# Performance work log

Hardware: AMD Instinct MI355X
Metric: run time of the kernel (lower is better)

Reference implementation:

```python
import jax, jax.numpy as jnp
import numpy as np

B, IC, OC, K, H, W = 8, 512, 512, 3, 32, 32
GAIN, LRMUL = 1.0, 1.0
# compute_runtime_coef: fan_in = prod(weight_shape[:-1])
RC_CONV = GAIN / np.sqrt(K * K * IC) * LRMUL   # conv weight [K,K,IC,OC]
RC_DENSE = GAIN / np.sqrt(IC) * LRMUL          # dense weight [IC, IC]


def setup_inputs() -> dict:
    key = jax.random.key(0)
    ks = jax.random.split(key, 4)
    x = jax.random.normal(ks[0], (B, IC, H, W), dtype=jnp.float32)
    w = jax.random.normal(ks[1], (B, IC), dtype=jnp.float32)
    # init_std = 1/lrmul = 1.0 for both weights; bias init zeros
    conv_w = jax.random.normal(ks[2], (K, K, IC, OC), dtype=jnp.float32)
    dense_w = jax.random.normal(ks[3], (IC, IC), dtype=jnp.float32)
    dense_b = jnp.zeros((IC,), dtype=jnp.float32)
    return {"x": x, "w": w, "conv_w": conv_w, "dense_w": dense_w, "dense_b": dense_b}


def reference(x, w, conv_w, dense_w, dense_b):
    b, ic, h, wd = x.shape
    # modulation: style = Dense(w) + bias + 1
    style = w @ (RC_DENSE * dense_w) + LRMUL * dense_b + 1.0        # [B, IC]
    wt = (RC_CONV * conv_w)[None] * style[:, None, None, :, None]   # [B,K,K,IC,OC]
    # demodulation: rsqrt of sum of squares over (kh, kw, ic)
    d = jax.lax.rsqrt(jnp.sum(jnp.square(wt), axis=(1, 2, 3)) + 1e-8)  # [B, OC]
    wt = wt * d[:, None, None, None, :]
    # grouped conv with groups = batch: weight -> OIHW [B*OC, IC, K, K]
    w_g = jnp.transpose(wt, (0, 4, 3, 1, 2)).reshape(b * OC, ic, K, K)
    xg = x.reshape(1, b * ic, h, wd)
    y = jax.lax.conv_general_dilated(
        xg, w_g, window_strides=(1, 1), padding="SAME",
        dimension_numbers=("NCHW", "OIHW", "NCHW"), feature_group_count=b)
    return y.reshape(b, OC, h, wd)
```

## Files before the change

### kernel.cpp

```cpp
#include <hip/hip_runtime.h>
#include <stdint.h>


#define B_   8
#define IC_  512
#define OC_  512

static constexpr float RC_DENSE = 0.04419417382415922f;
static constexpr float RC_CONV  = 0.014731391274719739f;

typedef _Float16 half8    __attribute__((ext_vector_type(8)));
typedef float    floatx16 __attribute__((ext_vector_type(16)));

__device__ __forceinline__ void g2l(const void* g, void* l) {
  __builtin_amdgcn_global_load_lds(
      (const __attribute__((address_space(1))) void*)g,
      (__attribute__((address_space(3))) void*)l, 16, 0, 0);
}

__global__ __launch_bounds__(256) void style_kernel(
    const float* __restrict__ wv, const float* __restrict__ dw,
    const float* __restrict__ db, float* __restrict__ sm,
    float* __restrict__ sm2) {
  const int b = blockIdx.y;
  const int i = blockIdx.x * 64 + (threadIdx.x & 63);
  const int jg = threadIdx.x >> 6;
  __shared__ float red[4][64];
  float p = 0.f;
  for (int j = jg * 128; j < jg * 128 + 128; ++j)
    p += wv[b * IC_ + j] * dw[(size_t)j * IC_ + i];
  red[jg][threadIdx.x & 63] = p;
  __syncthreads();
  if (threadIdx.x < 64) {
    float s = red[0][threadIdx.x] + red[1][threadIdx.x] +
              red[2][threadIdx.x] + red[3][threadIdx.x];
    s = s * RC_DENSE + db[i] + 1.0f;
    float v = s * RC_CONV;
    sm[b * IC_ + i] = v;
    sm2[b * IC_ + i] = v * v;
  }
}

__global__ __launch_bounds__(256) void prep_kernel(
    const float* __restrict__ cw, const float* __restrict__ x,
    const float* __restrict__ sm, const float* __restrict__ sm2,
    _Float16* __restrict__ Wtf, float* __restrict__ dpart,
    _Float16* __restrict__ xsp) {
  __shared__ __align__(16) char smem[33280];
  const int bid = blockIdx.x;
  const int tid = threadIdx.x;
  if (bid < 256) {
    _Float16* LA = (_Float16*)smem;
    float* redall = (float*)(smem + 18432);
    const int by2 = bid >> 4, icb = bid & 15;
    const int by = by2 >> 1, h2 = by2 & 1;
    const int oc0 = by * 64 + h2 * 32, ic0 = icb * 32;
    const int ocl = tid & 31, g = tid >> 5;
    float sq4[4] = {};
    for (int m = 0; m < 36; ++m) {
      int r = m * 8 + g;
      int t = r >> 5, icl = r & 31;
      float v = cw[(size_t)(t * IC_ + ic0 + icl) * OC_ + oc0 + ocl];
      sq4[m & 3] += v * v;
      LA[m * 256 + ocl * 8 + g] = (_Float16)v;
    }
    for (int b = 0; b < 8; ++b) {
      float p = 0.f;
      for (int s = 0; s < 4; ++s)
        p += sm2[b * IC_ + ic0 + g + 8 * s] * sq4[s];
      redall[(b * 8 + g) * 32 + ocl] = p;
    }
    __syncthreads();
    _Float16* dst = Wtf + (size_t)(by * 16 + icb) * 18432;
    for (int it = 0; it < 5; ++it) {
      int c = it * 256 + tid;
      if (c < 1152) {
        int m = c >> 5, o2 = c & 31;
        *(half8*)(dst + (size_t)(m * 64 + h2 * 32 + o2) * 8) =
            *(const half8*)&LA[m * 256 + o2 * 8];
      }
    }
    const int bb = tid >> 5, o3 = tid & 31;
    float s = 0.f;
    for (int g2 = 0; g2 < 8; ++g2) s += redall[(bb * 8 + g2) * 32 + o3];
    dpart[(size_t)icb * 4096 + bb * OC_ + oc0 + o3] = s;
  } else {
    _Float16* Xt = (_Float16*)smem;
    const int rb = bid - 256;
    const int b = rb >> 5, h = rb & 31;
    for (int k = 0; k < 16; ++k) {
      int idx = k * 256 + tid;
      int ic = idx >> 3, wc = (idx & 7) * 4;
      float4 v = *(const float4*)&x[((size_t)(b * IC_ + ic) * 32 + h) * 32 + wc];
      float s = sm[b * IC_ + ic];
      Xt[(wc + 0) * 520 + ic] = (_Float16)(v.x * s);
      Xt[(wc + 1) * 520 + ic] = (_Float16)(v.y * s);
      Xt[(wc + 2) * 520 + ic] = (_Float16)(v.z * s);
      Xt[(wc + 3) * 520 + ic] = (_Float16)(v.w * s);
    }
    __syncthreads();
    _Float16* xb = xsp + (size_t)b * 16 * 36992;
    const int r = h + 1;
    half8 z = {};
    for (int it = 0; it < 9; ++it) {
      int c = it * 256 + tid;
      if (c < 2176) {
        int icb = c / 136, rem = c - 136 * icb, kkq = rem / 34, C = rem - 34 * kkq;
        half8 val = z;
        if (C != 0 && C != 33)
          val = *(const half8*)&Xt[(C - 1) * 520 + icb * 32 + kkq * 8];
        *(half8*)&xb[(size_t)icb * 36992 + (size_t)r * 1088 + kkq * 272 + C * 8] = val;
      }
    }
    if (h == 0 || h == 31) {
      const int rz = (h == 0) ? 0 : 33;
      for (int it = 0; it < 9; ++it) {
        int c = it * 256 + tid;
        if (c < 2176) {
          int icb = c / 136, rem = c - 136 * icb, kkq = rem / 34, C = rem - 34 * kkq;
          *(half8*)&xb[(size_t)icb * 36992 + (size_t)rz * 1088 + kkq * 272 + C * 8] = z;
        }
      }
    }
  }
}

__global__ __launch_bounds__(512, 1) void conv_kernel(
    const _Float16* __restrict__ Wtf,
    const _Float16* __restrict__ xsp,
    const float* __restrict__ dpart,
    float* __restrict__ out) {
  extern __shared__ __align__(16) _Float16 dyn[];
  _Float16* As0 = dyn;
  _Float16* As1 = dyn + 18432;
  _Float16* Xs0 = dyn + 36864;
  _Float16* Xs1 = dyn + 47744;
  float* redd = (float*)(dyn + 58624);
  float* dvl  = redd + 512;

  const int by = blockIdx.x, bx = blockIdx.y, b = blockIdx.z;
  const int tid = threadIdx.x, lane = tid & 63, w = tid >> 6;
  const int wm = w & 1, wn = w >> 1;
  const int n = lane & 31, kq = lane >> 5;
  const int h0 = bx * 8;

  const _Float16* gA = Wtf + (size_t)(by * 16) * 18432;
  const _Float16* gX = xsp + (size_t)b * 16 * 36992 + (size_t)h0 * 1088;

  auto stage = [&](int icb, int p) {
    const _Float16* a  = gA + (size_t)icb * 18432;
    const _Float16* xg = gX + (size_t)icb * 36992;
    _Float16* Ad = p ? As1 : As0;
    _Float16* Xd = p ? Xs1 : Xs0;
#pragma unroll
    for (int k = 0; k < 4; ++k) {
      int c = w * 288 + k * 64 + lane;
      g2l(a + (size_t)c * 8, Ad + c * 8);
    }
    {
      int c = w * 288 + 256 + lane;
      if (lane < 32) g2l(a + (size_t)c * 8, Ad + c * 8);
    }
#pragma unroll
    for (int k = 0; k < 2; ++k) {
      int c = w * 170 + k * 64 + lane;
      g2l(xg + (size_t)c * 8, Xd + c * 8);
    }
    {
      int c = w * 170 + 128 + lane;
      if (lane < 42) g2l(xg + (size_t)c * 8, Xd + c * 8);
    }
  };

  floatx16 acc[2] = {};
  stage(0, 0);
  for (int st = 0; st < 16; ++st) {
    const int cur = st & 1;
    if (st + 1 < 16) {
      stage(st + 1, cur ^ 1);
      __builtin_amdgcn_sched_barrier(0);
      asm volatile("s_waitcnt vmcnt(8)" ::: "memory");
    } else {
      __builtin_amdgcn_sched_barrier(0);
      asm volatile("s_waitcnt vmcnt(0)" ::: "memory");
    }
    __builtin_amdgcn_s_barrier();
    __builtin_amdgcn_sched_barrier(0);
    const _Float16* Ar = (cur ? As1 : As0) + kq * 512 + wm * 256 + n * 8;
    const _Float16* Xr = (cur ? Xs1 : Xs0) + (2 * wn) * 1088 + kq * 272 + n * 8;
    half8 a[9][2];
#pragma unroll
    for (int t = 0; t < 9; ++t) {
      a[t][0] = *(const half8*)(Ar + (t * 4 + 0) * 512);
      a[t][1] = *(const half8*)(Ar + (t * 4 + 2) * 512);
    }
    __builtin_amdgcn_s_setprio(1);
#pragma unroll
    for (int kk = 0; kk < 2; ++kk) {
#pragma unroll
      for (int s = 0; s < 4; ++s) {
#pragma unroll
        for (int kw = 0; kw < 3; ++kw) {
          half8 xv = *(const half8*)(Xr + s * 1088 + kk * 544 + kw * 8);
#pragma unroll
          for (int kh = 0; kh < 3; ++kh) {
            int j = s - kh;
            if (j >= 0 && j < 2)
              acc[j] = __builtin_amdgcn_mfma_f32_32x32x16_f16(
                  a[kh * 3 + kw][kk], xv, acc[j], 0, 0, 0);
          }
        }
      }
    }
    __builtin_amdgcn_s_setprio(0);
    __builtin_amdgcn_sched_barrier(0);
    __builtin_amdgcn_s_barrier();
  }

  const int oc0 = by * 64 + wm * 32;
  __syncthreads();
  {
    const int oc_l = tid & 63, ig = tid >> 6;
    float s = dpart[(size_t)(ig * 2) * 4096 + b * OC_ + by * 64 + oc_l] +
              dpart[(size_t)(ig * 2 + 1) * 4096 + b * OC_ + by * 64 + oc_l];
    redd[ig * 64 + oc_l] = s;
  }
  __syncthreads();
  if (tid < 64) {
    float s = 1e-8f;
#pragma unroll
    for (int g = 0; g < 8; ++g) s += redd[g * 64 + tid];
    dvl[tid] = rsqrtf(s);
  }
  __syncthreads();
  const int r0 = h0 + 2 * wn;
#pragma unroll
  for (int rg = 0; rg < 16; ++rg) {
    const int row = (rg & 3) + 8 * (rg >> 2) + 4 * kq;
    const float dv = dvl[wm * 32 + row];
    float* op = out + ((size_t)b * OC_ + oc0 + row) * 1024 + r0 * 32 + n;
    op[0]  = acc[0][rg] * dv;
    op[32] = acc[1][rg] * dv;
  }
}

extern "C" void kernel_launch(void* const* d_in, const int* in_sizes, int n_in,
                              void* d_out, int out_size, void* d_ws, size_t ws_size,
                              hipStream_t stream) {
  const float* x       = (const float*)d_in[0];
  const float* w       = (const float*)d_in[1];
  const float* conv_w  = (const float*)d_in[2];
  const float* dense_w = (const float*)d_in[3];
  const float* dense_b = (const float*)d_in[4];
  float* out = (float*)d_out;

  char* ws = (char*)d_ws;
  float*    sm    = (float*)ws;
  float*    sm2   = (float*)(ws + (16 << 10));
  float*    dpart = (float*)(ws + (32 << 10));
  _Float16* Wtf   = (_Float16*)(ws + (288 << 10));
  _Float16* xsp   = (_Float16*)(ws + (288 << 10) + 4718592);

  static int dyn_set = 0;
  if (!dyn_set) {
    hipFuncSetAttribute((const void*)conv_kernel,
                        hipFuncAttributeMaxDynamicSharedMemorySize, 119552);
    dyn_set = 1;
  }

  style_kernel<<<dim3(8, B_), 256, 0, stream>>>(w, dense_w, dense_b, sm, sm2);
  prep_kernel<<<512, 256, 0, stream>>>(conv_w, x, sm, sm2, Wtf, dpart, xsp);
  conv_kernel<<<dim3(8, 4, B_), 512, 119552, stream>>>(Wtf, xsp, dpart, out);
}
```

Baseline: 129.3 us.

## Split conv mainloop into finer-grained multi-stage pipeline with interleaved LDS loads

Restructures the conv kernel's mainloop from a two-stage double buffer over whole IC blocks into a deeper pipeline over half-blocks (kk halves). Each block is now processed in four phases. Each phase issues a global-to-LDS copy for a stage ahead, preloads A/X fragments into registers, then runs its MFMAs, with waitcnt tuned per phase. The aim is to overlap memory transfers with MFMA work more evenly and shrink the register footprint of A fragments. The cost is more barriers per block and complex manual vmcnt bookkeeping that could race if miscounted.

```diff
diff --git a/kernel.cpp b/kernel.cpp
--- a/kernel.cpp
+++ b/kernel.cpp
@@ -125,16 +125,59 @@
   }
 }
 
+
+#define VM10 asm volatile("s_waitcnt vmcnt(10)" ::: "memory")
+#define VM5  asm volatile("s_waitcnt vmcnt(5)" ::: "memory")
+#define VM0  asm volatile("s_waitcnt vmcnt(0)" ::: "memory")
+#define VMNONE ((void)0)
+
+#define PHASE(KK, SH, PAR, DO_A, G2L_STMT, VM_STMT)                          \
+  {                                                                          \
+    if (DO_A) {                                                              \
+      const _Float16* Ad = dyn + ((KK) * 2 + (PAR)) * 9216 +                 \
+                           kq * 512 + wm * 256 + n * 8;                      \
+      _Pragma("unroll")                                                      \
+      for (int t_ = 0; t_ < 9; ++t_)                                         \
+        av[t_] = *(const half8*)(Ad + (t_ * 2) * 512);                       \
+    }                                                                        \
+    const _Float16* Xd = XB + ((KK) * 2 + (PAR)) * 5440 +                    \
+                         (2 * wn + 2 * (SH)) * 544 + kq * 272 + n * 8;       \
+    half8 xv0[3], xv1[3];                                                    \
+    _Pragma("unroll")                                                        \
+    for (int kw_ = 0; kw_ < 3; ++kw_) {                                      \
+      xv0[kw_] = *(const half8*)(Xd + kw_ * 8);                              \
+      xv1[kw_] = *(const half8*)(Xd + 544 + kw_ * 8);                        \
+    }                                                                        \
+    G2L_STMT;                                                                \
+    __builtin_amdgcn_s_barrier();                                            \
+    asm volatile("s_waitcnt lgkmcnt(0)" ::: "memory");                       \
+    __builtin_amdgcn_sched_barrier(0);                                       \
+    __builtin_amdgcn_s_setprio(1);                                           \
+    _Pragma("unroll")                                                        \
+    for (int kw_ = 0; kw_ < 3; ++kw_) {                                      \
+      if (SH == 0) {                                                         \
+        acc[0] = __builtin_amdgcn_mfma_f32_32x32x16_f16(av[0 + kw_], xv0[kw_], acc[0], 0, 0, 0); \
+        acc[1] = __builtin_amdgcn_mfma_f32_32x32x16_f16(av[0 + kw_], xv1[kw_], acc[1], 0, 0, 0); \
+        acc[0] = __builtin_amdgcn_mfma_f32_32x32x16_f16(av[3 + kw_], xv1[kw_], acc[0], 0, 0, 0); \
+      } else {                                                               \
+        acc[1] = __builtin_amdgcn_mfma_f32_32x32x16_f16(av[3 + kw_], xv0[kw_], acc[1], 0, 0, 0); \
+        acc[0] = __builtin_amdgcn_mfma_f32_32x32x16_f16(av[6 + kw_], xv0[kw_], acc[0], 0, 0, 0); \
+        acc[1] = __builtin_amdgcn_mfma_f32_32x32x16_f16(av[6 + kw_], xv1[kw_], acc[1], 0, 0, 0); \
+      }                                                                      \
+    }                                                                        \
+    __builtin_amdgcn_s_setprio(0);                                           \
+    __builtin_amdgcn_sched_barrier(0);                                       \
+    VM_STMT;                                                                 \
+    __builtin_amdgcn_s_barrier();                                            \
+  }
+
 __global__ __launch_bounds__(512, 1) void conv_kernel(
     const _Float16* __restrict__ Wtf,
     const _Float16* __restrict__ xsp,
     const float* __restrict__ dpart,
     float* __restrict__ out) {
   extern __shared__ __align__(16) _Float16 dyn[];
-  _Float16* As0 = dyn;
-  _Float16* As1 = dyn + 18432;
-  _Float16* Xs0 = dyn + 36864;
-  _Float16* Xs1 = dyn + 47744;
+  _Float16* XB = dyn + 36864;
   float* redd = (float*)(dyn + 58624);
   float* dvl  = redd + 512;
 
@@ -147,75 +190,68 @@
   const _Float16* gA = Wtf + (size_t)(by * 16) * 18432;
   const _Float16* gX = xsp + (size_t)b * 16 * 36992 + (size_t)h0 * 1088;
 
-  auto stage = [&](int icb, int p) {
-    const _Float16* a  = gA + (size_t)icb * 18432;
-    const _Float16* xg = gX + (size_t)icb * 36992;
-    _Float16* Ad = p ? As1 : As0;
-    _Float16* Xd = p ? Xs1 : Xs0;
-#pragma unroll
-    for (int k = 0; k < 4; ++k) {
-      int c = w * 288 + k * 64 + lane;
-      g2l(a + (size_t)c * 8, Ad + c * 8);
-    }
-    {
-      int c = w * 288 + 256 + lane;
-      if (lane < 32) g2l(a + (size_t)c * 8, Ad + c * 8);
-    }
+  auto stageA3 = [&](int g) {
+    const int icb = g >> 1, kk = g & 1, par = icb & 1;
+    const _Float16* a = gA + (size_t)icb * 18432;
+    _Float16* Ad = dyn + (kk * 2 + par) * 9216;
 #pragma unroll
     for (int k = 0; k < 2; ++k) {
-      int c = w * 170 + k * 64 + lane;
-      g2l(xg + (size_t)c * 8, Xd + c * 8);
+      int c = w * 144 + k * 64 + lane;
+      int mi = c >> 6, o = c & 63;
+      int m = (mi >> 1) * 4 + kk * 2 + (mi & 1);
+      g2l(a + (size_t)(m * 512 + o * 8), Ad + c * 8);
     }
     {
-      int c = w * 170 + 128 + lane;
-      if (lane < 42) g2l(xg + (size_t)c * 8, Xd + c * 8);
+      int c = w * 144 + 128 + lane;
+      if (lane < 16) {
+        int mi = c >> 6, o = c & 63;
+        int m = (mi >> 1) * 4 + kk * 2 + (mi & 1);
+        g2l(a + (size_t)(m * 512 + o * 8), Ad + c * 8);
+      }
     }
   };
+  auto stageX2 = [&](int g) {
+    const int icb = g >> 1, kk = g & 1, par = icb & 1;
+    const _Float16* xg = gX + (size_t)icb * 36992 + kk * 544;
+    _Float16* Xd = XB + (kk * 2 + par) * 5440;
+    {
+      int c = w * 85 + lane;
+      int r = c / 68, o = c - r * 68;
+      g2l(xg + (size_t)(r * 1088 + o * 8), Xd + c * 8);
+    }
+    {
+      int c = w * 85 + 64 + lane;
+      if (lane < 21) {
+        int r = c / 68, o = c - r * 68;
+        g2l(xg + (size_t)(r * 1088 + o * 8), Xd + c * 8);
+      }
+    }
+  };
 
   floatx16 acc[2] = {};
-  stage(0, 0);
-  for (int st = 0; st < 16; ++st) {
-    const int cur = st & 1;
-    if (st + 1 < 16) {
-      stage(st + 1, cur ^ 1);
-      __builtin_amdgcn_sched_barrier(0);
-      asm volatile("s_waitcnt vmcnt(8)" ::: "memory");
-    } else {
-      __builtin_amdgcn_sched_barrier(0);
-      asm volatile("s_waitcnt vmcnt(0)" ::: "memory");
-    }
-    __builtin_amdgcn_s_barrier();
-    __builtin_amdgcn_sched_barrier(0);
-    const _Float16* Ar = (cur ? As1 : As0) + kq * 512 + wm * 256 + n * 8;
-    const _Float16* Xr = (cur ? Xs1 : Xs0) + (2 * wn) * 1088 + kq * 272 + n * 8;
-    half8 a[9][2];
-#pragma unroll
-    for (int t = 0; t < 9; ++t) {
-      a[t][0] = *(const half8*)(Ar + (t * 4 + 0) * 512);
-      a[t][1] = *(const half8*)(Ar + (t * 4 + 2) * 512);
-    }
-    __builtin_amdgcn_s_setprio(1);
-#pragma unroll
-    for (int kk = 0; kk < 2; ++kk) {
-#pragma unroll
-      for (int s = 0; s < 4; ++s) {
-#pragma unroll
-        for (int kw = 0; kw < 3; ++kw) {
-          half8 xv = *(const half8*)(Xr + s * 1088 + kk * 544 + kw * 8);
-#pragma unroll
-          for (int kh = 0; kh < 3; ++kh) {
-            int j = s - kh;
-            if (j >= 0 && j < 2)
-              acc[j] = __builtin_amdgcn_mfma_f32_32x32x16_f16(
-                  a[kh * 3 + kw][kk], xv, acc[j], 0, 0, 0);
-          }
-        }
-      }
-    }
-    __builtin_amdgcn_s_setprio(0);
-    __builtin_amdgcn_sched_barrier(0);
-    __builtin_amdgcn_s_barrier();
-  }
+  half8 av[9];
+  stageA3(0); stageX2(0);
+  stageA3(1); stageX2(1);
+  stageA3(2); stageX2(2);
+  VM10;
+  __builtin_amdgcn_s_barrier();
+
+  for (int st = 0; st < 14; ++st) {
+    const int par = st & 1;
+    const int g3 = 2 * st + 3, g4 = 2 * st + 4;
+    PHASE(0, 0, par, true,  stageA3(g3), VMNONE)
+    PHASE(0, 1, par, false, stageX2(g3), VM10)
+    PHASE(1, 0, par, true,  stageA3(g4), VMNONE)
+    PHASE(1, 1, par, false, stageX2(g4), VM10)
+  }
+  PHASE(0, 0, 0, true,  stageA3(31), VMNONE)
+  PHASE(0, 1, 0, false, stageX2(31), VM10)
+  PHASE(1, 0, 0, true,  VMNONE, VMNONE)
+  PHASE(1, 1, 0, false, VMNONE, VM5)
+  PHASE(0, 0, 1, true,  VMNONE, VMNONE)
+  PHASE(0, 1, 1, false, VMNONE, VM0)
+  PHASE(1, 0, 1, true,  VMNONE, VMNONE)
+  PHASE(1, 1, 1, false, VMNONE, VMNONE)
 
   const int oc0 = by * 64 + wm * 32;
   __syncthreads();
```

New measurement: 127.5 us, median of 2. Within noise of the previous version (-1.4%).
